# Performance work log

Measured on AMD Instinct MI355X. Metric: run time of the kernel, lower is better.

Reference implementation:

```python
import jax, jax.numpy as jnp
import numpy as np

B, N, D = 4, 2048, 1024
H = 16
HD = D // H


def setup_inputs() -> dict:
    key = jax.random.key(0)
    ks = jax.random.split(key, 6)
    x = jax.random.normal(ks[0], (B, N, D), dtype=jnp.float32)
    # additive causal mask: 0 on/below diagonal, -inf above
    neg = jnp.float32(-1e9)
    causal_mask = jnp.where(jnp.triu(jnp.ones((N, N), dtype=bool), k=1), neg, 0.0).astype(jnp.float32)
    s = 1.0 / np.sqrt(D)
    Wqkv = jax.random.normal(ks[1], (D, 3 * D), dtype=jnp.float32) * s
    bqkv = jax.random.normal(ks[2], (3 * D,), dtype=jnp.float32) * 0.01
    Wproj = jax.random.normal(ks[3], (D, D), dtype=jnp.float32) * s
    bproj = jax.random.normal(ks[4], (D,), dtype=jnp.float32) * 0.01
    return {"x": x, "causal_mask": causal_mask, "Wqkv": Wqkv, "bqkv": bqkv, "Wproj": Wproj, "bproj": bproj}


def reference(x, causal_mask, Wqkv, bqkv, Wproj, bproj):
    b, n, d = x.shape
    qkv = x @ Wqkv + bqkv  # [B,N,3D]
    qkv = qkv.reshape(b, n, 3, H, HD).transpose(2, 0, 3, 1, 4)  # [3,B,H,N,HD]
    q, k, v = qkv[0], qkv[1], qkv[2]
    scale = HD ** -0.5
    attn = jnp.einsum('bhqd,bhkd->bhqk', q, k) * scale  # [B,H,N,N]
    attn = attn + causal_mask  # broadcast [N,N] -> [B,H,N,N]
    attn = jax.nn.softmax(attn, axis=-1)
    out = jnp.einsum('bhqk,bhkd->bhqd', attn, v)  # [B,H,N,HD]
    out = out.transpose(0, 2, 1, 3).reshape(b, n, d)
    return out @ Wproj + bproj
```

## Files before the change

kernel.cpp:

```cpp
#include <hip/hip_runtime.h>
#include <hip/hip_bf16.h>

typedef unsigned short u16;
typedef unsigned int u32;
typedef __attribute__((ext_vector_type(8))) short bf16x8;
typedef __attribute__((ext_vector_type(4))) float f32x4;
typedef __attribute__((ext_vector_type(16))) float f32x16;

#define AS1(p) ((const __attribute__((address_space(1))) void*)(p))
#define AS3(p) ((__attribute__((address_space(3))) void*)(p))
#define STG(src, dst) __builtin_amdgcn_global_load_lds(AS1(src), AS3(dst), 16, 0, 0)

#if __has_builtin(__builtin_amdgcn_exp2f)
#define EXP2F(x) __builtin_amdgcn_exp2f(x)
#else
#define EXP2F(x) exp2f(x)
#endif

static __device__ __forceinline__ float b2f(u16 u) {
  union { unsigned int i; float f; } v; v.i = ((unsigned int)u) << 16; return v.f;
}
static __device__ __forceinline__ u16 f2b(float f) {
  union { float f; unsigned int i; } v; v.f = f;
  unsigned int r = v.i + 0x7FFFu + ((v.i >> 16) & 1u);
  return (u16)(r >> 16);
}
static __device__ __forceinline__ u32 cvt_pk_bf16(float lo, float hi) {
  u32 r;
  asm("v_cvt_pk_bf16_f32 %0, %1, %2" : "=v"(r) : "v"(lo), "v"(hi));
  return r;
}
static __device__ __forceinline__ void permswap(u32& a, u32& b) {
  asm("v_permlane32_swap_b32 %0, %1" : "+v"(a), "+v"(b));
}

__global__ __launch_bounds__(256) void cast_f32_bf16(const float* __restrict__ src,
                                                     u16* __restrict__ dst, int n8) {
  int stride = gridDim.x * blockDim.x;
  for (int i = blockIdx.x * blockDim.x + threadIdx.x; i < n8; i += stride) {
    const float4* s = (const float4*)(src + (size_t)i * 8);
    float4 a = s[0], b = s[1];
    bf16x8 o;
    o[0] = (short)f2b(a.x); o[1] = (short)f2b(a.y); o[2] = (short)f2b(a.z); o[3] = (short)f2b(a.w);
    o[4] = (short)f2b(b.x); o[5] = (short)f2b(b.y); o[6] = (short)f2b(b.z); o[7] = (short)f2b(b.w);
    *(bf16x8*)(dst + (size_t)i * 8) = o;
  }
}

__global__ __launch_bounds__(256) void transpose_w(const float* __restrict__ src,
                                                   u16* __restrict__ dst,
                                                   int R, int C) {
  __shared__ float tile[32][33];
  int c0 = blockIdx.x * 32, r0 = blockIdx.y * 32;
  int tx = threadIdx.x, ty = threadIdx.y;
  for (int i = ty; i < 32; i += 8) tile[i][tx] = src[(size_t)(r0 + i) * C + c0 + tx];
  __syncthreads();
  for (int i = ty; i < 32; i += 8) dst[(size_t)(c0 + i) * R + r0 + tx] = f2b(tile[tx][i]);
}

__global__ __launch_bounds__(256) void transpose_v(const u16* __restrict__ qkv,
                                                   u16* __restrict__ VT) {
  const int N = 2048, TD = 3072, D = 1024;
  int bh = blockIdx.y, n0 = blockIdx.x * 64;
  int b = bh >> 4, h = bh & 15;
  int tid = threadIdx.x;
  __shared__ u16 tl[64][72];
  #pragma unroll
  for (int i = 0; i < 16; ++i) {
    int idx = tid + i * 256;
    int nl = idx >> 6, dd = idx & 63;
    tl[dd][nl] = qkv[(size_t)(b * N + n0 + nl) * TD + 2 * D + h * 64 + dd];
  }
  __syncthreads();
  #pragma unroll
  for (int i = 0; i < 16; ++i) {
    int idx = tid + i * 256;
    int dd = idx >> 6, nl = idx & 63;
    VT[((size_t)bh * 64 + dd) * N + n0 + nl] = tl[dd][nl];
  }
}

template <typename OutT>
__global__ __launch_bounds__(256, 2) void gemm256(
    const u16* __restrict__ A,
    const u16* __restrict__ BT,
    const float* __restrict__ bias,
    OutT* __restrict__ C,
    int M, int N, int K, int nn) {
  __shared__ alignas(16) u16 As[2][256 * 32];
  __shared__ alignas(16) u16 Bs[2][128 * 32];

  const int nwg = gridDim.x, cpx = nwg >> 3, id0 = blockIdx.x;
  const int swz = (id0 & 7) * cpx + (id0 >> 3);
  const int mi = swz / nn, ni = swz % nn;
  const int m0 = mi * 256, n0 = ni * 128;

  const int t = threadIdx.x;
  const int wid = t >> 6, lane = t & 63;
  const int wr = wid >> 1, wc = wid & 1;
  const int rlo = lane & 15, g = lane >> 4;

  const u16* aSrc[4];
  const u16* bSrc[2];
  int dA[4], dB[2];
  #pragma unroll
  for (int k = 0; k < 4; ++k) {
    const int c = t + 256 * k, cs = c ^ ((c >> 3) & 3);
    aSrc[k] = A + (size_t)(m0 + (cs >> 2)) * K + (cs & 3) * 8;
    dA[k] = c * 8;
  }
  #pragma unroll
  for (int k = 0; k < 2; ++k) {
    const int c = t + 256 * k, cs = c ^ ((c >> 3) & 3);
    bSrc[k] = BT + (size_t)(n0 + (cs >> 2)) * K + (cs & 3) * 8;
    dB[k] = c * 8;
  }

  f32x4 acc[8][4] = {};
  const int NT = K >> 5;

  #pragma unroll
  for (int k = 0; k < 4; ++k) STG(aSrc[k], &As[0][dA[k]]);
  #pragma unroll
  for (int k = 0; k < 2; ++k) STG(bSrc[k], &Bs[0][dB[k]]);

  for (int kt = 0; kt < NT; ++kt) {
    const int db = kt & 1;
    __syncthreads();

    if (kt + 1 < NT) {
      const int nx = db ^ 1, ko = (kt + 1) * 32;
      #pragma unroll
      for (int k = 0; k < 4; ++k) STG(aSrc[k] + ko, &As[nx][dA[k]]);
      #pragma unroll
      for (int k = 0; k < 2; ++k) STG(bSrc[k] + ko, &Bs[nx][dB[k]]);
    }

    const char* aB = (const char*)&As[db][0];
    const char* bB = (const char*)&Bs[db][0];
    bf16x8 a[8], b[4];
    #pragma unroll
    for (int fr = 0; fr < 8; ++fr) {
      const int r_ = wr * 128 + fr * 16 + rlo;
      a[fr] = *(const bf16x8*)(aB + (r_ * 64 + ((g ^ ((r_ >> 1) & 3)) << 4)));
    }
    #pragma unroll
    for (int fn = 0; fn < 4; ++fn) {
      const int r_ = wc * 64 + fn * 16 + rlo;
      b[fn] = *(const bf16x8*)(bB + (r_ * 64 + ((g ^ ((r_ >> 1) & 3)) << 4)));
    }
    __builtin_amdgcn_s_setprio(1);
    #pragma unroll
    for (int fr = 0; fr < 8; ++fr)
      #pragma unroll
      for (int fn = 0; fn < 4; ++fn)
        acc[fr][fn] = __builtin_amdgcn_mfma_f32_16x16x32_bf16(a[fr], b[fn], acc[fr][fn], 0, 0, 0);
    __builtin_amdgcn_s_setprio(0);
  }

  #pragma unroll
  for (int fn = 0; fn < 4; ++fn) {
    const int col = n0 + wc * 64 + fn * 16 + rlo;
    const float bv = bias[col];
    #pragma unroll
    for (int fr = 0; fr < 8; ++fr) {
      const int row = m0 + wr * 128 + fr * 16 + g * 4;
      #pragma unroll
      for (int i = 0; i < 4; ++i) {
        float r = acc[fr][fn][i] + bv;
        if constexpr (sizeof(OutT) == 2)
          C[(size_t)(row + i) * N + col] = (OutT)f2b(r);
        else
          C[(size_t)(row + i) * N + col] = (OutT)r;
      }
    }
  }
}

__global__ __launch_bounds__(256) void attn_fwd(
    const u16* __restrict__ qkv,
    const u16* __restrict__ VT,
    u16* __restrict__ O) {
  const int N = 2048, TD = 3072, D = 1024;
  const int bid = blockIdx.x;
  const int qp = bid >> 6, bh = bid & 63;
  const int b = bh >> 4, h = bh & 15;
  const int t = threadIdx.x, w = t >> 6, lane = t & 63;
  const int l31 = lane & 31, hi = lane >> 5;

  __shared__ alignas(16) u16 Kls[64 * 64];
  __shared__ alignas(16) u16 Vls[64 * 64];

  const int c1 = t, c2 = t + 256;
  const int r1 = c1 >> 3, sc1 = ((c1 & 7) ^ (r1 & 7)) * 8;
  const int r2 = c2 >> 3, sc2 = ((c2 & 7) ^ (r2 & 7)) * 8;
  const u16* kbase = qkv + (size_t)(b * N) * TD + D + h * 64;
  const u16* vbase = VT + (size_t)bh * 64 * N;

  const float L2E = 1.44269504089f;
  const float NSH = -23.0830992f;

  for (int pass = 0; pass < 2; ++pass) {
    const int qt = pass ? (15 - qp) : qp;
    const int qbase = qt * 128 + w * 32;

    bf16x8 qf[4];
    {
      const u16* qp_ = qkv + ((size_t)(b * N) + qbase + l31) * TD + h * 64 + hi * 8;
      #pragma unroll
      for (int c = 0; c < 4; ++c) {
        bf16x8 v = *(const bf16x8*)(qp_ + c * 16);
        #pragma unroll
        for (int j = 0; j < 8; ++j)
          v[j] = (short)f2b(b2f((u16)v[j]) * 0.125f);
        qf[c] = v;
      }
    }

    f32x16 o_acc[2] = {};
    float psum = 0.f;
    const int jend = qt * 128 + 64;

    for (int j0 = 0; j0 <= jend; j0 += 64) {
      STG(kbase + (size_t)(j0 + r1) * TD + sc1, &Kls[c1 * 8]);
      STG(kbase + (size_t)(j0 + r2) * TD + sc2, &Kls[c2 * 8]);
      STG(vbase + (size_t)r1 * N + j0 + sc1, &Vls[c1 * 8]);
      STG(vbase + (size_t)r2 * N + j0 + sc2, &Vls[c2 * 8]);
      __syncthreads();

      if (j0 <= qbase + 31) {
        bf16x8 kf[2][4];
        #pragma unroll
        for (int st = 0; st < 2; ++st) {
          const int row = st * 32 + l31, sw = (row & 7) << 3;
          #pragma unroll
          for (int c = 0; c < 4; ++c)
            kf[st][c] = *(const bf16x8*)&Kls[row * 64 + ((c * 16 + hi * 8) ^ sw)];
        }
        bf16x8 vf[2][2][2];
        #pragma unroll
        for (int dt = 0; dt < 2; ++dt) {
          const int row = dt * 32 + l31, sw = (row & 7) << 3;
          #pragma unroll
          for (int st = 0; st < 2; ++st)
            #pragma unroll
            for (int kc = 0; kc < 2; ++kc)
              vf[st][kc][dt] = *(const bf16x8*)&Vls[row * 64 + ((st * 32 + kc * 16 + hi * 8) ^ sw)];
        }

        const int qr = qbase + l31;
        const bool straddle = !(j0 + 63 <= qbase);
        #pragma unroll
        for (int st = 0; st < 2; ++st) {
          if (st == 1 && !(j0 < qbase)) continue;
          f32x16 S = {};
          __builtin_amdgcn_s_setprio(1);
          #pragma unroll
          for (int c = 0; c < 4; ++c)
            S = __builtin_amdgcn_mfma_f32_32x32x16_bf16(kf[st][c], qf[c], S, 0, 0, 0);
          __builtin_amdgcn_s_setprio(0);
          if (straddle) {
            const int kvb = j0 + st * 32 + 4 * hi;
            #pragma unroll
            for (int r = 0; r < 16; ++r)
              if (kvb + (r & 3) + 8 * (r >> 2) > qr) S[r] = -1e30f;
          }
          float p[16];
          #pragma unroll
          for (int r = 0; r < 16; ++r) p[r] = EXP2F(fmaf(S[r], L2E, NSH));
          float ps = 0.f;
          #pragma unroll
          for (int r = 0; r < 16; ++r) ps += p[r];
          psum += ps;
          u32 wq[8];
          #pragma unroll
          for (int i = 0; i < 8; ++i) wq[i] = cvt_pk_bf16(p[2 * i], p[2 * i + 1]);
          permswap(wq[0], wq[2]); permswap(wq[1], wq[3]);
          permswap(wq[4], wq[6]); permswap(wq[5], wq[7]);
          union { u32 u[4]; bf16x8 v; } pa0, pa1;
          pa0.u[0] = wq[0]; pa0.u[1] = wq[1]; pa0.u[2] = wq[2]; pa0.u[3] = wq[3];
          pa1.u[0] = wq[4]; pa1.u[1] = wq[5]; pa1.u[2] = wq[6]; pa1.u[3] = wq[7];
          __builtin_amdgcn_s_setprio(1);
          #pragma unroll
          for (int dt = 0; dt < 2; ++dt) {
            o_acc[dt] = __builtin_amdgcn_mfma_f32_32x32x16_bf16(pa0.v, vf[st][0][dt], o_acc[dt], 0, 0, 0);
            o_acc[dt] = __builtin_amdgcn_mfma_f32_32x32x16_bf16(pa1.v, vf[st][1][dt], o_acc[dt], 0, 0, 0);
          }
          __builtin_amdgcn_s_setprio(0);
        }
      }
      __syncthreads();
    }

    float rs = psum + __shfl_xor(psum, 32, 64);
    float inv = 1.0f / rs;
    #pragma unroll
    for (int r = 0; r < 16; ++r) {
      const int qrow = (r & 3) + 8 * (r >> 2) + 4 * hi;
      const float invq = __shfl(inv, qrow, 64);
      const int q = qbase + qrow;
      #pragma unroll
      for (int dt = 0; dt < 2; ++dt)
        O[((size_t)(b * N) + q) * D + h * 64 + dt * 32 + l31] = f2b(o_acc[dt][r] * invq);
    }
  }
}

extern "C" void kernel_launch(void* const* d_in, const int* in_sizes, int n_in,
                              void* d_out, int out_size, void* d_ws, size_t ws_size,
                              hipStream_t stream) {
  const float* x     = (const float*)d_in[0];
  const float* Wqkv  = (const float*)d_in[2];
  const float* bqkv  = (const float*)d_in[3];
  const float* Wproj = (const float*)d_in[4];
  const float* bproj = (const float*)d_in[5];
  float* out = (float*)d_out;

  const int B = 4, N = 2048, D = 1024, H = 16;
  const int BN = B * N;
  const int TD = 3 * D;

  char* ws = (char*)d_ws;
  u16* qkv    = (u16*)(ws);
  u16* vt     = (u16*)(ws + 50331648);
  u16* aout   = (u16*)(ws + 67108864);
  u16* wqkvT  = (u16*)(ws + 83886080);
  u16* wprojT = (u16*)(ws + 90177536);
  u16* xb     = (u16*)(ws + 92274688);

  cast_f32_bf16<<<2048, 256, 0, stream>>>(x, xb, BN * D / 8);
  transpose_w<<<dim3(TD / 32, D / 32), dim3(32, 8), 0, stream>>>(Wqkv, wqkvT, D, TD);
  transpose_w<<<dim3(D / 32, D / 32), dim3(32, 8), 0, stream>>>(Wproj, wprojT, D, D);
  gemm256<u16><<<768, 256, 0, stream>>>(xb, wqkvT, bqkv, qkv, BN, TD, D, 24);
  transpose_v<<<dim3(N / 64, B * H), 256, 0, stream>>>(qkv, vt);
  attn_fwd<<<512, 256, 0, stream>>>(qkv, vt, aout);
  gemm256<float><<<256, 256, 0, stream>>>(aout, wprojT, bproj, out, BN, D, D, 8);
}
```

Measured before the change: 203.2 us.

## Split attention waves across KV halves with LDS reduction of partial outputs

Each wave previously owned 32 query rows and processed both 32-key sub-tiles. Now wave pairs share 64 query rows and each wave handles one 32-key half of every KV tile. Partial outputs and row sums are merged through LDS, reusing the K/V pool buffers, at the end of each pass. This is meant to balance causal-mask work across waves and let each wave reuse its K fragment against two query blocks. It also sets launch_bounds to 2 blocks per SM, at the cost of extra reduction syncs and doubled accumulator registers.

```diff
diff --git a/kernel.cpp b/kernel.cpp
--- a/kernel.cpp
+++ b/kernel.cpp
@@ -177,7 +177,7 @@
   }
 }
 
-__global__ __launch_bounds__(256) void attn_fwd(
+__global__ __launch_bounds__(256, 2) void attn_fwd(
     const u16* __restrict__ qkv,
     const u16* __restrict__ VT,
     u16* __restrict__ O) {
@@ -187,9 +187,11 @@
   const int b = bh >> 4, h = bh & 15;
   const int t = threadIdx.x, w = t >> 6, lane = t & 63;
   const int l31 = lane & 31, hi = lane >> 5;
-
-  __shared__ alignas(16) u16 Kls[64 * 64];
-  __shared__ alignas(16) u16 Vls[64 * 64];
+  const int qh = w >> 1, st = w & 1;
+
+  __shared__ alignas(16) u16 pool16[2][64 * 64];
+  __shared__ float rsLds[2][32];
+  float* poolf = (float*)&pool16[0][0];
 
   const int c1 = t, c2 = t + 256;
   const int r1 = c1 >> 3, sc1 = ((c1 & 7) ^ (r1 & 7)) * 8;
@@ -202,65 +204,63 @@
 
   for (int pass = 0; pass < 2; ++pass) {
     const int qt = pass ? (15 - qp) : qp;
-    const int qbase = qt * 128 + w * 32;
-
-    bf16x8 qf[4];
-    {
-      const u16* qp_ = qkv + ((size_t)(b * N) + qbase + l31) * TD + h * 64 + hi * 8;
+    const int qbw = qt * 128 + qh * 64;
+
+    bf16x8 qf[2][4];
+    #pragma unroll
+    for (int qs = 0; qs < 2; ++qs) {
+      const u16* qp_ = qkv + ((size_t)(b * N) + qbw + qs * 32 + l31) * TD + h * 64 + hi * 8;
       #pragma unroll
       for (int c = 0; c < 4; ++c) {
         bf16x8 v = *(const bf16x8*)(qp_ + c * 16);
         #pragma unroll
         for (int j = 0; j < 8; ++j)
           v[j] = (short)f2b(b2f((u16)v[j]) * 0.125f);
-        qf[c] = v;
-      }
-    }
-
-    f32x16 o_acc[2] = {};
-    float psum = 0.f;
+        qf[qs][c] = v;
+      }
+    }
+
+    f32x16 o_acc[2][2] = {};
+    float psum[2] = {0.f, 0.f};
     const int jend = qt * 128 + 64;
 
     for (int j0 = 0; j0 <= jend; j0 += 64) {
-      STG(kbase + (size_t)(j0 + r1) * TD + sc1, &Kls[c1 * 8]);
-      STG(kbase + (size_t)(j0 + r2) * TD + sc2, &Kls[c2 * 8]);
-      STG(vbase + (size_t)r1 * N + j0 + sc1, &Vls[c1 * 8]);
-      STG(vbase + (size_t)r2 * N + j0 + sc2, &Vls[c2 * 8]);
+      STG(kbase + (size_t)(j0 + r1) * TD + sc1, &pool16[0][c1 * 8]);
+      STG(kbase + (size_t)(j0 + r2) * TD + sc2, &pool16[0][c2 * 8]);
+      STG(vbase + (size_t)r1 * N + j0 + sc1, &pool16[1][c1 * 8]);
+      STG(vbase + (size_t)r2 * N + j0 + sc2, &pool16[1][c2 * 8]);
       __syncthreads();
 
-      if (j0 <= qbase + 31) {
-        bf16x8 kf[2][4];
-        #pragma unroll
-        for (int st = 0; st < 2; ++st) {
+      const int sb = j0 + st * 32;
+      if (sb <= qbw + 63) {
+        bf16x8 kf[4];
+        {
           const int row = st * 32 + l31, sw = (row & 7) << 3;
           #pragma unroll
           for (int c = 0; c < 4; ++c)
-            kf[st][c] = *(const bf16x8*)&Kls[row * 64 + ((c * 16 + hi * 8) ^ sw)];
+            kf[c] = *(const bf16x8*)&pool16[0][row * 64 + ((c * 16 + hi * 8) ^ sw)];
         }
-        bf16x8 vf[2][2][2];
+        bf16x8 vf[2][2];
         #pragma unroll
         for (int dt = 0; dt < 2; ++dt) {
           const int row = dt * 32 + l31, sw = (row & 7) << 3;
           #pragma unroll
-          for (int st = 0; st < 2; ++st)
-            #pragma unroll
-            for (int kc = 0; kc < 2; ++kc)
-              vf[st][kc][dt] = *(const bf16x8*)&Vls[row * 64 + ((st * 32 + kc * 16 + hi * 8) ^ sw)];
+          for (int kc = 0; kc < 2; ++kc)
+            vf[kc][dt] = *(const bf16x8*)&pool16[1][row * 64 + ((st * 32 + kc * 16 + hi * 8) ^ sw)];
         }
 
-        const int qr = qbase + l31;
-        const bool straddle = !(j0 + 63 <= qbase);
-        #pragma unroll
-        for (int st = 0; st < 2; ++st) {
-          if (st == 1 && !(j0 < qbase)) continue;
+        #pragma unroll
+        for (int qs = 0; qs < 2; ++qs) {
+          if (qs == 0 && sb > qbw + 31) continue;
+          const int qr = qbw + qs * 32 + l31;
           f32x16 S = {};
           __builtin_amdgcn_s_setprio(1);
           #pragma unroll
           for (int c = 0; c < 4; ++c)
-            S = __builtin_amdgcn_mfma_f32_32x32x16_bf16(kf[st][c], qf[c], S, 0, 0, 0);
+            S = __builtin_amdgcn_mfma_f32_32x32x16_bf16(kf[c], qf[qs][c], S, 0, 0, 0);
           __builtin_amdgcn_s_setprio(0);
-          if (straddle) {
-            const int kvb = j0 + st * 32 + 4 * hi;
+          if (sb + 31 > qbw + qs * 32) {
+            const int kvb = sb + 4 * hi;
             #pragma unroll
             for (int r = 0; r < 16; ++r)
               if (kvb + (r & 3) + 8 * (r >> 2) > qr) S[r] = -1e30f;
@@ -271,7 +271,7 @@
           float ps = 0.f;
           #pragma unroll
           for (int r = 0; r < 16; ++r) ps += p[r];
-          psum += ps;
+          psum[qs] += ps;
           u32 wq[8];
           #pragma unroll
           for (int i = 0; i < 8; ++i) wq[i] = cvt_pk_bf16(p[2 * i], p[2 * i + 1]);
@@ -283,8 +283,8 @@
           __builtin_amdgcn_s_setprio(1);
           #pragma unroll
           for (int dt = 0; dt < 2; ++dt) {
-            o_acc[dt] = __builtin_amdgcn_mfma_f32_32x32x16_bf16(pa0.v, vf[st][0][dt], o_acc[dt], 0, 0, 0);
-            o_acc[dt] = __builtin_amdgcn_mfma_f32_32x32x16_bf16(pa1.v, vf[st][1][dt], o_acc[dt], 0, 0, 0);
+            o_acc[qs][dt] = __builtin_amdgcn_mfma_f32_32x32x16_bf16(pa0.v, vf[0][dt], o_acc[qs][dt], 0, 0, 0);
+            o_acc[qs][dt] = __builtin_amdgcn_mfma_f32_32x32x16_bf16(pa1.v, vf[1][dt], o_acc[qs][dt], 0, 0, 0);
           }
           __builtin_amdgcn_s_setprio(0);
         }
@@ -292,16 +292,37 @@
       __syncthreads();
     }
 
-    float rs = psum + __shfl_xor(psum, 32, 64);
-    float inv = 1.0f / rs;
-    #pragma unroll
-    for (int r = 0; r < 16; ++r) {
-      const int qrow = (r & 3) + 8 * (r >> 2) + 4 * hi;
-      const float invq = __shfl(inv, qrow, 64);
-      const int q = qbase + qrow;
-      #pragma unroll
-      for (int dt = 0; dt < 2; ++dt)
-        O[((size_t)(b * N) + q) * D + h * 64 + dt * 32 + l31] = f2b(o_acc[dt][r] * invq);
+    float rsown[2];
+    #pragma unroll
+    for (int qs = 0; qs < 2; ++qs)
+      rsown[qs] = psum[qs] + __shfl_xor(psum[qs], 32, 64);
+
+    #pragma unroll
+    for (int qs = 0; qs < 2; ++qs) {
+      if (st != qs) {
+        #pragma unroll
+        for (int dt = 0; dt < 2; ++dt)
+          #pragma unroll
+          for (int r = 0; r < 16; ++r)
+            poolf[qh * 2048 + (dt * 16 + r) * 64 + lane] = o_acc[qs][dt][r];
+        rsLds[qh][l31] = rsown[qs];
+      }
+      __syncthreads();
+      if (st == qs) {
+        const float inv = 1.0f / (rsown[qs] + rsLds[qh][l31]);
+        #pragma unroll
+        for (int r = 0; r < 16; ++r) {
+          const int qrow = (r & 3) + 8 * (r >> 2) + 4 * hi;
+          const float invq = __shfl(inv, qrow, 64);
+          const int q = qbw + qs * 32 + qrow;
+          #pragma unroll
+          for (int dt = 0; dt < 2; ++dt) {
+            const float val = o_acc[qs][dt][r] + poolf[qh * 2048 + (dt * 16 + r) * 64 + lane];
+            O[((size_t)(b * N) + q) * D + h * 64 + dt * 32 + l31] = f2b(val * invq);
+          }
+        }
+      }
+      __syncthreads();
     }
   }
 }
```

New measurement: 194.9 us. 4.1% less time.
